# Performance work log

Hardware: AMD Instinct MI355X
Metric: run time of the kernel (lower is better)

The kernel has to match this reference:

```python
import jax, jax.numpy as jnp
import numpy as np

# NF4 (NormalFloat4) codebook from QLoRA / bitsandbytes
NF4_TABLE = jnp.array([
    -1.0, -0.6961928009986877, -0.5250730514526367, -0.39491748809814453,
    -0.28444138169288635, -0.18477343022823334, -0.09105003625154495, 0.0,
    0.07958029955625534, 0.16093020141124725, 0.24611230194568634,
    0.33791524171829224, 0.44070982933044434, 0.5626170039176941,
    0.7229568362236023, 1.0], dtype=jnp.float32)

IN_FEATURES = 4096
OUT_FEATURES = 11008
BLOCKSIZE = 64
NUMEL = IN_FEATURES * OUT_FEATURES          # 45_088_768
PACKED = NUMEL // 2                          # 22_544_384
NBLOCKS = NUMEL // BLOCKSIZE                 # 704_512


def setup_inputs() -> dict:
    key = jax.random.key(0)
    k1, k2, k3, k4 = jax.random.split(key, 4)
    x = jax.random.normal(k1, (2048, IN_FEATURES), dtype=jnp.float32)
    # packed uint8 codes, stored as int32 in [0, 256)
    packed = jax.random.randint(k2, (PACKED,), 0, 256, dtype=jnp.int32)
    # per-block absmax scales (positive)
    absmax = jax.random.uniform(k3, (NBLOCKS,), dtype=jnp.float32, minval=0.01, maxval=1.0)
    bias = jax.random.normal(k4, (OUT_FEATURES,), dtype=jnp.float32)
    return {"x": x, "packed": packed, "absmax": absmax, "bias": bias}


def _dequantize_nf4(packed, absmax):
    # unpack two 4-bit codes per byte: high nibble first, then low nibble
    hi = packed >> 4            # [P]
    lo = packed & 0xF           # [P]
    codes = jnp.stack([hi, lo], axis=-1).reshape(-1)       # [numel]
    vals = jnp.take(NF4_TABLE, codes)                      # [numel]
    # per-block absmax scaling
    w = (vals.reshape(-1, BLOCKSIZE) * absmax[:, None]).reshape(OUT_FEATURES, IN_FEATURES)
    return w


def reference(x, packed, absmax, bias):
    w = _dequantize_nf4(packed, absmax)                    # [out, in]
    # y = x @ W^T + b
    return jnp.einsum('ti,oi->to', x, w) + bias[None, :]
```

## Files before the change

### kernel.cpp

```cpp
#include <hip/hip_runtime.h>
#include <hip/hip_bf16.h>


#define IN_F   4096
#define OUT_F  11008
#define M_ROWS 2048
#define BM 128
#define BN 128
#define BK 64
#define LDSS 72

typedef short  s16x8 __attribute__((ext_vector_type(8)));
typedef unsigned short u16x8 __attribute__((ext_vector_type(8)));
typedef float  f32x4 __attribute__((ext_vector_type(4)));
typedef int    i32x4 __attribute__((ext_vector_type(4)));
typedef unsigned int u32x4 __attribute__((ext_vector_type(4)));

__device__ const float NF4_C[16] = {
    -1.0f, -0.6961928009986877f, -0.5250730514526367f, -0.39491748809814453f,
    -0.28444138169288635f, -0.18477343022823334f, -0.09105003625154495f, 0.0f,
    0.07958029955625534f, 0.16093020141124725f, 0.24611230194568634f,
    0.33791524171829224f, 0.44070982933044434f, 0.5626170039176941f,
    0.7229568362236023f, 1.0f};

static __device__ __forceinline__ unsigned short f2bf(float f) {
    union { float f; unsigned int u; } c;
    c.f = f;
    unsigned int u = c.u;
    u += 0x7fffu + ((u >> 16) & 1u);
    return (unsigned short)(u >> 16);
}

static __device__ __forceinline__ void gload_lds16(const void* g, void* l) {
    __builtin_amdgcn_global_load_lds(
        (const __attribute__((address_space(1))) void*)g,
        (__attribute__((address_space(3))) void*)l, 16, 0, 0);
}

#define DQ_BLOCKS 11008
#define CV_BLOCKS 4096

__global__ __launch_bounds__(256)
void prep_kernel(const float* __restrict__ x,
                 const int* __restrict__ packed,
                 const float* __restrict__ absmax,
                 unsigned short* __restrict__ xb,
                 unsigned short* __restrict__ wb) {
    if (blockIdx.x < DQ_BLOCKS) {
        __shared__ float2 tab[256];
        tab[threadIdx.x] = make_float2(NF4_C[threadIdx.x >> 4], NF4_C[threadIdx.x & 15]);
        __syncthreads();

        const size_t t = (size_t)blockIdx.x * 256 + threadIdx.x;
        const i32x4* p = reinterpret_cast<const i32x4*>(packed) + t * 2;
        i32x4 a = __builtin_nontemporal_load(p);
        i32x4 b = __builtin_nontemporal_load(p + 1);
        const float s = absmax[t >> 2];

        int vs[8] = {a[0], a[1], a[2], a[3], b[0], b[1], b[2], b[3]};
        unsigned int ow[8];
#pragma unroll
        for (int j = 0; j < 8; ++j) {
            float2 tv = tab[vs[j] & 0xFF];
            ow[j] = (unsigned int)f2bf(tv.x * s) | ((unsigned int)f2bf(tv.y * s) << 16);
        }
        u32x4* dst = reinterpret_cast<u32x4*>(wb + t * 16);
        dst[0] = (u32x4){ow[0], ow[1], ow[2], ow[3]};
        dst[1] = (u32x4){ow[4], ow[5], ow[6], ow[7]};
    } else {
        const size_t t = (size_t)(blockIdx.x - DQ_BLOCKS) * 256 + threadIdx.x;
        const f32x4* src = reinterpret_cast<const f32x4*>(x) + t * 2;
        f32x4 v0 = __builtin_nontemporal_load(src);
        f32x4 v1 = __builtin_nontemporal_load(src + 1);
        u16x8 o;
        o[0] = f2bf(v0[0]); o[1] = f2bf(v0[1]); o[2] = f2bf(v0[2]); o[3] = f2bf(v0[3]);
        o[4] = f2bf(v1[0]); o[5] = f2bf(v1[1]); o[6] = f2bf(v1[2]); o[7] = f2bf(v1[3]);
        *reinterpret_cast<u16x8*>(xb + t * 8) = o;
    }
}

__global__ __launch_bounds__(256, 2)
void gemm_bt_kernel(const unsigned short* __restrict__ xb,
                    const unsigned short* __restrict__ wb,
                    const float* __restrict__ bias,
                    float* __restrict__ out) {
    __shared__ __align__(16) unsigned short As[BM * BK];
    __shared__ __align__(16) unsigned short Bs[BN * BK];

    const int tid  = threadIdx.x;
    const int lane = tid & 63;
    const int wave = tid >> 6;
    const int quad = lane >> 4;
    const int l16  = lane & 15;
    const int wm = wave & 1;
    const int wn = wave >> 1;

    const int mBase = blockIdx.x * BM;
    const int nBase = blockIdx.y * BN;

    const int srow = tid >> 3;
    const int scol = (tid & 7) * 8;

    f32x4 acc[4][4];
#pragma unroll
    for (int mi = 0; mi < 4; ++mi)
#pragma unroll
        for (int ni = 0; ni < 4; ++ni)
            acc[mi][ni] = (f32x4){0.f, 0.f, 0.f, 0.f};

    const unsigned short* aSrc = xb + (size_t)(mBase + srow) * IN_F + scol;
    const unsigned short* bSrc = wb + (size_t)(nBase + srow) * IN_F + scol;

    for (int kt = 0; kt < IN_F / BK; ++kt) {
        const int k0 = kt * BK;
        __syncthreads();
#pragma unroll
        for (int i = 0; i < 4; ++i)
            gload_lds16(aSrc + (size_t)i * 32 * IN_F + k0, &As[(i * 32 + srow) * BK + scol]);
#pragma unroll
        for (int i = 0; i < 4; ++i)
            gload_lds16(bSrc + (size_t)i * 32 * IN_F + k0, &Bs[(i * 32 + srow) * BK + scol]);
        __syncthreads();

#pragma unroll
        for (int kk = 0; kk < 2; ++kk) {
            const int kof = kk * 32 + quad * 8;
            s16x8 af[4], bfr[4];
#pragma unroll
            for (int mi = 0; mi < 4; ++mi)
                af[mi] = *reinterpret_cast<const s16x8*>(
                    &As[(wm * 64 + mi * 16 + l16) * BK + kof]);
#pragma unroll
            for (int ni = 0; ni < 4; ++ni)
                bfr[ni] = *reinterpret_cast<const s16x8*>(
                    &Bs[(wn * 64 + ni * 16 + l16) * BK + kof]);
#pragma unroll
            for (int mi = 0; mi < 4; ++mi)
#pragma unroll
                for (int ni = 0; ni < 4; ++ni)
                    acc[mi][ni] = __builtin_amdgcn_mfma_f32_16x16x32_bf16(
                        af[mi], bfr[ni], acc[mi][ni], 0, 0, 0);
        }
    }

    float bv[4];
#pragma unroll
    for (int ni = 0; ni < 4; ++ni)
        bv[ni] = bias[nBase + wn * 64 + ni * 16 + l16];
#pragma unroll
    for (int mi = 0; mi < 4; ++mi) {
        const int rbase = mBase + wm * 64 + mi * 16 + quad * 4;
#pragma unroll
        for (int ni = 0; ni < 4; ++ni) {
            const int col = nBase + wn * 64 + ni * 16 + l16;
#pragma unroll
            for (int r = 0; r < 4; ++r)
                __builtin_nontemporal_store(acc[mi][ni][r] + bv[ni],
                    &out[(size_t)(rbase + r) * OUT_F + col]);
        }
    }
}

__global__ __launch_bounds__(256, 2)
void nf4_linear_fused(const float* __restrict__ x,
                      const int* __restrict__ packed,
                      const float* __restrict__ absmax,
                      const float* __restrict__ bias,
                      float* __restrict__ out) {
    __shared__ __align__(16) unsigned short As[BM * LDSS];
    __shared__ __align__(16) unsigned short Bs[BN * LDSS];
    __shared__ float2 tab[256];

    const int tid  = threadIdx.x;
    const int lane = tid & 63;
    const int wave = tid >> 6;
    const int quad = lane >> 4;
    const int l16  = lane & 15;
    const int wm = wave & 1;
    const int wn = wave >> 1;
    const int mBase = blockIdx.y * BM;
    const int nBase = blockIdx.x * BN;

    tab[tid] = make_float2(NF4_C[tid >> 4], NF4_C[tid & 15]);

    f32x4 acc[4][4];
#pragma unroll
    for (int mi = 0; mi < 4; ++mi)
#pragma unroll
        for (int ni = 0; ni < 4; ++ni)
            acc[mi][ni] = (f32x4){0.f, 0.f, 0.f, 0.f};

    const int brow  = tid >> 1;
    const int bhalf = tid & 1;
    const int ng    = nBase + brow;

    for (int kt = 0; kt < IN_F / BK; ++kt) {
        const int k0 = kt * BK;
        __syncthreads();
#pragma unroll
        for (int i = 0; i < 4; ++i) {
            int gid = tid + i * 256;
            int row = gid >> 3;
            int c8  = gid & 7;
            const float4* src = reinterpret_cast<const float4*>(
                x + (size_t)(mBase + row) * IN_F + k0 + c8 * 8);
            float4 v0 = src[0];
            float4 v1 = src[1];
            u16x8 o;
            o[0] = f2bf(v0.x); o[1] = f2bf(v0.y); o[2] = f2bf(v0.z); o[3] = f2bf(v0.w);
            o[4] = f2bf(v1.x); o[5] = f2bf(v1.y); o[6] = f2bf(v1.z); o[7] = f2bf(v1.w);
            *reinterpret_cast<u16x8*>(&As[row * LDSS + c8 * 8]) = o;
        }
        {
            const float scale = absmax[(size_t)ng * 64 + (k0 >> 6)];
            const int4* bp = reinterpret_cast<const int4*>(
                packed + (size_t)ng * (IN_F / 2) + (k0 >> 1) + bhalf * 16);
            const int colw = bhalf * 32;
#pragma unroll
            for (int c = 0; c < 4; ++c) {
                int4 v = bp[c];
                int vs[4] = {v.x, v.y, v.z, v.w};
                unsigned int ow[4];
#pragma unroll
                for (int j = 0; j < 4; ++j) {
                    float2 t = tab[vs[j] & 0xFF];
                    ow[j] = (unsigned int)f2bf(t.x * scale)
                          | ((unsigned int)f2bf(t.y * scale) << 16);
                }
                *reinterpret_cast<uint4*>(&Bs[brow * LDSS + colw + c * 8]) =
                    *reinterpret_cast<const uint4*>(ow);
            }
        }
        __syncthreads();

#pragma unroll
        for (int kk = 0; kk < 2; ++kk) {
            const int kof = kk * 32 + quad * 8;
            s16x8 af[4], bfr[4];
#pragma unroll
            for (int mi = 0; mi < 4; ++mi)
                af[mi] = *reinterpret_cast<const s16x8*>(
                    &As[(wm * 64 + mi * 16 + l16) * LDSS + kof]);
#pragma unroll
            for (int ni = 0; ni < 4; ++ni)
                bfr[ni] = *reinterpret_cast<const s16x8*>(
                    &Bs[(wn * 64 + ni * 16 + l16) * LDSS + kof]);
#pragma unroll
            for (int mi = 0; mi < 4; ++mi)
#pragma unroll
                for (int ni = 0; ni < 4; ++ni)
                    acc[mi][ni] = __builtin_amdgcn_mfma_f32_16x16x32_bf16(
                        af[mi], bfr[ni], acc[mi][ni], 0, 0, 0);
        }
    }

    float bv[4];
#pragma unroll
    for (int ni = 0; ni < 4; ++ni)
        bv[ni] = bias[nBase + wn * 64 + ni * 16 + l16];
#pragma unroll
    for (int mi = 0; mi < 4; ++mi) {
        const int rbase = mBase + wm * 64 + mi * 16 + quad * 4;
#pragma unroll
        for (int ni = 0; ni < 4; ++ni) {
            const int col = nBase + wn * 64 + ni * 16 + l16;
#pragma unroll
            for (int r = 0; r < 4; ++r)
                out[(size_t)(rbase + r) * OUT_F + col] = acc[mi][ni][r] + bv[ni];
        }
    }
}

extern "C" void kernel_launch(void* const* d_in, const int* in_sizes, int n_in,
                              void* d_out, int out_size, void* d_ws, size_t ws_size,
                              hipStream_t stream) {
    const float* x      = (const float*)d_in[0];
    const int*   packed = (const int*)d_in[1];
    const float* absmax = (const float*)d_in[2];
    const float* bias   = (const float*)d_in[3];
    float* out = (float*)d_out;

    const size_t xb_bytes = (size_t)M_ROWS * IN_F * 2;
    const size_t wb_bytes = (size_t)OUT_F * IN_F * 2;
    if (ws_size >= xb_bytes + wb_bytes) {
        unsigned short* xb = (unsigned short*)d_ws;
        unsigned short* wb = (unsigned short*)((char*)d_ws + xb_bytes);
        prep_kernel<<<dim3(DQ_BLOCKS + CV_BLOCKS), dim3(256), 0, stream>>>(
            x, packed, absmax, xb, wb);
        gemm_bt_kernel<<<dim3(M_ROWS / BM, OUT_F / BN), dim3(256), 0, stream>>>(
            xb, wb, bias, out);
    } else {
        nf4_linear_fused<<<dim3(OUT_F / BN, M_ROWS / BM), dim3(256), 0, stream>>>(
            x, packed, absmax, bias, out);
    }
}
```

Before: 396.2 us.

## Swizzle GEMM LDS layout via XOR on global source and restructure prep loads

The GEMM's direct-to-LDS loads now fetch a global column chunk XOR-swizzled by row, while reads use the matching XOR index. This removes LDS bank conflicts on the 16-byte fragment reads of the unpadded 64-element rows. The prep kernel is also reorganised so each thread does two coalesced 16-byte units spaced 256 apart, with split hi/lo lookup tables instead of one strided 32-byte access. The swizzle keeps the data the same and only changes which global chunk lands in each LDS slot.

```diff
diff --git a/kernel.cpp b/kernel.cpp
--- a/kernel.cpp
+++ b/kernel.cpp
@@ -47,35 +47,39 @@
                  unsigned short* __restrict__ xb,
                  unsigned short* __restrict__ wb) {
     if (blockIdx.x < DQ_BLOCKS) {
-        __shared__ float2 tab[256];
-        tab[threadIdx.x] = make_float2(NF4_C[threadIdx.x >> 4], NF4_C[threadIdx.x & 15]);
-        __syncthreads();
-
-        const size_t t = (size_t)blockIdx.x * 256 + threadIdx.x;
-        const i32x4* p = reinterpret_cast<const i32x4*>(packed) + t * 2;
-        i32x4 a = __builtin_nontemporal_load(p);
-        i32x4 b = __builtin_nontemporal_load(p + 1);
-        const float s = absmax[t >> 2];
-
-        int vs[8] = {a[0], a[1], a[2], a[3], b[0], b[1], b[2], b[3]};
-        unsigned int ow[8];
-#pragma unroll
-        for (int j = 0; j < 8; ++j) {
-            float2 tv = tab[vs[j] & 0xFF];
-            ow[j] = (unsigned int)f2bf(tv.x * s) | ((unsigned int)f2bf(tv.y * s) << 16);
-        }
-        u32x4* dst = reinterpret_cast<u32x4*>(wb + t * 16);
-        dst[0] = (u32x4){ow[0], ow[1], ow[2], ow[3]};
-        dst[1] = (u32x4){ow[4], ow[5], ow[6], ow[7]};
+        __shared__ float tab_hi[256];
+        __shared__ float tab_lo[256];
+        tab_hi[threadIdx.x] = NF4_C[threadIdx.x >> 4];
+        tab_lo[threadIdx.x] = NF4_C[threadIdx.x & 15];
+        __syncthreads();
+
+        const size_t u0 = (size_t)blockIdx.x * 512 + threadIdx.x;
+#pragma unroll
+        for (int h = 0; h < 2; ++h) {
+            const size_t u = u0 + h * 256;
+            i32x4 v = __builtin_nontemporal_load(
+                reinterpret_cast<const i32x4*>(packed) + u);
+            const float s = absmax[u >> 3];
+            unsigned int ow[4];
+#pragma unroll
+            for (int j = 0; j < 4; ++j) {
+                const int b = v[j] & 0xFF;
+                ow[j] = (unsigned int)f2bf(tab_hi[b] * s)
+                      | ((unsigned int)f2bf(tab_lo[b] * s) << 16);
+            }
+            *(reinterpret_cast<u32x4*>(wb) + u) = (u32x4){ow[0], ow[1], ow[2], ow[3]};
+        }
     } else {
-        const size_t t = (size_t)(blockIdx.x - DQ_BLOCKS) * 256 + threadIdx.x;
-        const f32x4* src = reinterpret_cast<const f32x4*>(x) + t * 2;
-        f32x4 v0 = __builtin_nontemporal_load(src);
-        f32x4 v1 = __builtin_nontemporal_load(src + 1);
-        u16x8 o;
-        o[0] = f2bf(v0[0]); o[1] = f2bf(v0[1]); o[2] = f2bf(v0[2]); o[3] = f2bf(v0[3]);
-        o[4] = f2bf(v1[0]); o[5] = f2bf(v1[1]); o[6] = f2bf(v1[2]); o[7] = f2bf(v1[3]);
-        *reinterpret_cast<u16x8*>(xb + t * 8) = o;
+        const size_t u0 = (size_t)(blockIdx.x - DQ_BLOCKS) * 512 + threadIdx.x;
+#pragma unroll
+        for (int h = 0; h < 2; ++h) {
+            const size_t u = u0 + h * 256;
+            f32x4 v = __builtin_nontemporal_load(
+                reinterpret_cast<const f32x4*>(x) + u);
+            ushort4 o;
+            o.x = f2bf(v[0]); o.y = f2bf(v[1]); o.z = f2bf(v[2]); o.w = f2bf(v[3]);
+            *(reinterpret_cast<ushort4*>(xb) + u) = o;
+        }
     }
 }
 
@@ -99,7 +103,8 @@
     const int nBase = blockIdx.y * BN;
 
     const int srow = tid >> 3;
-    const int scol = (tid & 7) * 8;
+    const int sc   = tid & 7;
+    const int scS  = sc ^ (srow & 7);
 
     f32x4 acc[4][4];
 #pragma unroll
@@ -108,32 +113,35 @@
         for (int ni = 0; ni < 4; ++ni)
             acc[mi][ni] = (f32x4){0.f, 0.f, 0.f, 0.f};
 
-    const unsigned short* aSrc = xb + (size_t)(mBase + srow) * IN_F + scol;
-    const unsigned short* bSrc = wb + (size_t)(nBase + srow) * IN_F + scol;
+    const unsigned short* aSrc = xb + (size_t)(mBase + srow) * IN_F + scS * 8;
+    const unsigned short* bSrc = wb + (size_t)(nBase + srow) * IN_F + scS * 8;
+
+    const int sw = l16 & 7;
 
     for (int kt = 0; kt < IN_F / BK; ++kt) {
         const int k0 = kt * BK;
         __syncthreads();
 #pragma unroll
         for (int i = 0; i < 4; ++i)
-            gload_lds16(aSrc + (size_t)i * 32 * IN_F + k0, &As[(i * 32 + srow) * BK + scol]);
+            gload_lds16(aSrc + (size_t)i * 32 * IN_F + k0, &As[(i * 32 + srow) * BK + sc * 8]);
 #pragma unroll
         for (int i = 0; i < 4; ++i)
-            gload_lds16(bSrc + (size_t)i * 32 * IN_F + k0, &Bs[(i * 32 + srow) * BK + scol]);
+            gload_lds16(bSrc + (size_t)i * 32 * IN_F + k0, &Bs[(i * 32 + srow) * BK + sc * 8]);
         __syncthreads();
 
 #pragma unroll
         for (int kk = 0; kk < 2; ++kk) {
-            const int kof = kk * 32 + quad * 8;
+            const int q  = kk * 4 + quad;
+            const int rd = (q ^ sw) * 8;
             s16x8 af[4], bfr[4];
 #pragma unroll
             for (int mi = 0; mi < 4; ++mi)
                 af[mi] = *reinterpret_cast<const s16x8*>(
-                    &As[(wm * 64 + mi * 16 + l16) * BK + kof]);
+                    &As[(wm * 64 + mi * 16 + l16) * BK + rd]);
 #pragma unroll
             for (int ni = 0; ni < 4; ++ni)
                 bfr[ni] = *reinterpret_cast<const s16x8*>(
-                    &Bs[(wn * 64 + ni * 16 + l16) * BK + kof]);
+                    &Bs[(wn * 64 + ni * 16 + l16) * BK + rd]);
 #pragma unroll
             for (int mi = 0; mi < 4; ++mi)
 #pragma unroll
```

After: 348.2 us. 12.1% less time.
